# Kernel optimization log

Hardware: AMD Instinct MI355X
Metric: run time of the kernel (lower is better)

Reference implementation:

```python
import jax, jax.numpy as jnp
import numpy as np

N = 20000      # nodes
D_IN = 512     # input_dim
D_H = 256      # hyper_dim = input_dim // 2
C = 7          # class_num
E = 320000     # edges per class graph
E2 = 100000    # candidate pair list length
B = 8192       # batch of evaluated pairs (edge_id)
H3 = D_IN + C * D_H  # 2304, GatedNetwork / fc2 width
MIN = 1e-15
CURV = 1.0

def _norm(x):
    return jnp.maximum(jnp.linalg.norm(x, axis=-1, keepdims=True), MIN)

def artanh(x):
    x = jnp.clip(x, -1.0 + 1e-7, 1.0 - 1e-7)
    return 0.5 * (jnp.log1p(x) - jnp.log1p(-x))

def proj(x, c):
    # clip to inside the Poincare ball
    n = _norm(x)
    maxn = (1.0 - 4e-3) / jnp.sqrt(c)
    return jnp.where(n > maxn, x / n * maxn, x)

def expmap0(u, c):
    sc = jnp.sqrt(c); n = _norm(u)
    return jnp.tanh(sc * n) * u / (sc * n)

def logmap0(p, c):
    sc = jnp.sqrt(c); n = _norm(p)
    return artanh(sc * n) * p / (sc * n)

def mobius_add(x, y, c):
    x2 = jnp.sum(x * x, -1, keepdims=True)
    y2 = jnp.sum(y * y, -1, keepdims=True)
    xy = jnp.sum(x * y, -1, keepdims=True)
    num = (1 + 2 * c * xy + c * y2) * x + (1 - c * x2) * y
    den = 1 + 2 * c * xy + c * c * x2 * y2
    return num / jnp.maximum(den, MIN)

def mobius_matvec(m, x, c):
    sc = jnp.sqrt(c)
    xn = _norm(x)
    mx = x @ m.T
    mxn = _norm(mx)
    res = jnp.tanh(mxn / xn * artanh(sc * xn)) * mx / (mxn * sc)
    zero = jnp.all(mx == 0, axis=-1, keepdims=True)
    return jnp.where(zero, jnp.zeros((), mx.dtype), res)


def setup_inputs() -> dict:
    key = jax.random.key(0)
    ks = iter(jax.random.split(key, 48))
    def dense(shape, fan_in):
        return jax.random.normal(next(ks), shape, jnp.float32) * (1.0 / np.sqrt(fan_in))
    inp = {}
    inp['f1'] = jax.random.normal(next(ks), (N, D_IN), jnp.float32)
    inp['adj_src'] = jax.random.randint(next(ks), (C, E), 0, N)
    inp['adj_dst'] = jax.random.randint(next(ks), (C, E), 0, N)
    inp['adj_val'] = jax.random.uniform(next(ks), (C, E), jnp.float32) / 16.0  # ~row-normalized weights
    inp['edge_src'] = jax.random.randint(next(ks), (C, E), 0, N)
    inp['edge_dst'] = jax.random.randint(next(ks), (C, E), 0, N)
    inp['edge_index'] = jax.random.randint(next(ks), (2, E2), 0, N)
    inp['edge_id'] = jax.random.randint(next(ks), (B,), 0, E2)
    # per-class HypLinear
    inp['W_hyp'] = dense((C, D_H, D_IN), D_IN)
    inp['b_hyp'] = jnp.zeros((C, D_H), jnp.float32)
    # per-class HyperbolicDecoder linear
    inp['Wd'] = dense((C, D_H, D_H), D_H)
    inp['bd'] = jnp.zeros((C, D_H), jnp.float32)
    # per-class GIN MLP: lin1 -> BN -> tanh -> lin2
    inp['Wg1'] = dense((C, D_H, D_H), D_H)
    inp['bg1'] = jnp.zeros((C, D_H), jnp.float32)
    inp['gamma'] = jnp.ones((C, D_H), jnp.float32)
    inp['beta'] = jnp.zeros((C, D_H), jnp.float32)
    inp['Wg2'] = dense((C, D_H, D_H), D_H)
    inp['bg2'] = jnp.zeros((C, D_H), jnp.float32)
    # GatedInteractionNetwork
    inp['Wgate'] = dense((H3, H3), H3); inp['bgate'] = jnp.zeros((H3,), jnp.float32)
    inp['Wint'] = dense((H3, H3), H3); inp['bint'] = jnp.zeros((H3,), jnp.float32)
    inp['Wout'] = dense((H3, H3), H3); inp['bout'] = jnp.zeros((H3,), jnp.float32)
    # fc2 MLP head
    inp['Wf1'] = dense((H3 // 2, H3), H3); inp['bf1'] = jnp.zeros((H3 // 2,), jnp.float32)
    inp['Wf2'] = dense((H3 // 4, H3 // 2), H3 // 2); inp['bf2'] = jnp.zeros((H3 // 4,), jnp.float32)
    inp['Wf3'] = dense((C, H3 // 4), H3 // 4); inp['bf3'] = jnp.zeros((C,), jnp.float32)
    return inp


def reference(f1, adj_val, W_hyp, b_hyp, Wd, bd, Wg1, bg1, gamma, beta, Wg2, bg2,
              Wgate, bgate, Wint, bint, Wout, bout, Wf1, bf1, Wf2, bf2, Wf3, bf3,
              adj_src, adj_dst, edge_src, edge_dst, edge_index, edge_id):
    c = jnp.float32(CURV)
    # proj_tan0 is identity on the Poincare ball
    x_hyp = proj(expmap0(f1, c), c)
    outs = [f1]
    for i in range(C):
        # HypLinear: mobius matvec + hyperbolic bias
        res = proj(mobius_matvec(W_hyp[i], x_hyp, c), c)
        hb = proj(expmap0(b_hyp[i][None, :], c), c)
        res = proj(mobius_add(res, hb, c), c)
        # HypAgg: spmm(adj, logmap0(x)) then expmap0
        xt = logmap0(res, c)                     # [N, D_H]
        msg = adj_val[i][:, None] * xt[adj_src[i]]
        support = jax.ops.segment_sum(msg, adj_dst[i], num_segments=N)
        h = proj(expmap0(support, c), c)
        # HypAct: relu in tangent space at origin
        h = proj(expmap0(jax.nn.relu(logmap0(h, c)), c), c)
        # HyperbolicDecoder: logmap0 then euclidean linear
        d = logmap0(h, c) @ Wd[i].T + bd[i]
        # GIN (1 layer, eps=0): mlp(x + sum_neighbors x_j), mlp = lin->BN->tanh->lin
        agg = d + jax.ops.segment_sum(d[edge_src[i]], edge_dst[i], num_segments=N)
        z = agg @ Wg1[i].T + bg1[i]
        mu = jnp.mean(z, axis=0)
        var = jnp.var(z, axis=0)
        z = (z - mu) / jnp.sqrt(var + 1e-5) * gamma[i] + beta[i]
        z = jnp.tanh(z)
        outs.append(z @ Wg2[i].T + bg2[i])
    x = jnp.concatenate(outs, axis=1)            # [N, H3]
    nid = edge_index[:, edge_id]                 # [2, B]
    x1 = x[nid[0]]
    x2 = x[nid[1]]
    # GatedInteractionNetwork
    gate = jax.nn.sigmoid((x1 + x2) @ Wgate.T + bgate)
    gi = gate * jax.nn.relu((x1 * x2) @ Wint.T + bint)
    g = gi @ Wout.T + bout
    # fc2 head
    h1 = jax.nn.relu(g @ Wf1.T + bf1)
    h2 = jax.nn.relu(h1 @ Wf2.T + bf2)
    return h2 @ Wf3.T + bf3                      # [B, C]
```

## Files before the change

### kernel.cpp

```cpp
#include <hip/hip_runtime.h>
#include <math.h>

#define N_NODES 20000
#define D_INN   512
#define DH      256
#define NCH     7
#define NE      320000
#define NE2     100000
#define NB      8192
#define H3      2304
#define MAXN    0.996f
#define LOG2E   1.44269504f
#define NBUK    40
#define BSH     9

typedef unsigned short u16;
typedef __attribute__((ext_vector_type(8))) short bf16x8;
typedef __attribute__((ext_vector_type(4))) float f32x4;

__device__ __forceinline__ u16 f2b(float f) {
    unsigned int x = __float_as_uint(f);
    unsigned int r = (x + 0x7fffu + ((x >> 16) & 1u)) >> 16;
    return (u16)r;
}
__device__ __forceinline__ float b2f(u16 u) {
    return __uint_as_float(((unsigned int)u) << 16);
}
__device__ __forceinline__ float blo(unsigned int u) { return __uint_as_float(u << 16); }
__device__ __forceinline__ float bhi(unsigned int u) { return __uint_as_float(u & 0xffff0000u); }
__device__ __forceinline__ unsigned int pk2(float a, float b) {
    return (unsigned int)f2b(a) | ((unsigned int)f2b(b) << 16);
}

__device__ __forceinline__ float rcp_f(float x) { return __builtin_amdgcn_rcpf(x); }
__device__ __forceinline__ float exp2_f(float x) { return __builtin_amdgcn_exp2f(x); }
__device__ __forceinline__ float log2_f(float x) { return __builtin_amdgcn_logf(x); }
__device__ __forceinline__ float tanh_fast(float x) {
    float xc = fminf(fmaxf(x, -15.f), 15.f);
    float t = exp2_f(xc * (2.f * LOG2E));
    return (t - 1.f) * rcp_f(t + 1.f);
}
__device__ __forceinline__ float artanh_fast(float x) {
    x = fminf(fmaxf(x, -1.0f + 1e-7f), 1.0f - 1e-7f);
    return 0.34657359f * log2_f((1.f + x) * rcp_f(1.f - x));
}
__device__ __forceinline__ float sigmoid_fast(float x) {
    return rcp_f(1.f + exp2_f(-x * LOG2E));
}

__device__ __forceinline__ float wave_sum(float v) {
    #pragma unroll
    for (int off = 32; off > 0; off >>= 1) v += __shfl_xor(v, off, 64);
    return v;
}

__device__ __forceinline__ float block_sum256(float v) {
    __shared__ float sred[4];
    #pragma unroll
    for (int off = 32; off > 0; off >>= 1) v += __shfl_down(v, off, 64);
    int lane = threadIdx.x & 63;
    int w = threadIdx.x >> 6;
    if (lane == 0) sred[w] = v;
    __syncthreads();
    float tot = sred[0] + sred[1] + sred[2] + sred[3];
    __syncthreads();
    return tot;
}

__global__ void k_zero(float* __restrict__ p, int n) {
    int i = blockIdx.x * 256 + threadIdx.x;
    if (i < n) p[i] = 0.0f;
}
__global__ void k_izero(int* __restrict__ p, int n) {
    int i = blockIdx.x * 256 + threadIdx.x;
    if (i < n) p[i] = 0;
}

__global__ void k_f2b(const float* __restrict__ s, u16* __restrict__ d, int n4) {
    int i = blockIdx.x * 256 + threadIdx.x;
    int stride = gridDim.x * 256;
    for (; i < n4; i += stride) {
        float4 v = ((const float4*)s)[i];
        uint2 o; o.x = pk2(v.x, v.y); o.y = pk2(v.z, v.w);
        ((uint2*)d)[i] = o;
    }
}

__global__ void k_bias2(const float* __restrict__ a, const float* __restrict__ b,
                        float* __restrict__ o) {
    int i = blockIdx.x * 256 + threadIdx.x;
    if (i < H3) o[i] = a[i];
    else if (i < 2 * H3) o[i] = b[i - H3];
}

__global__ void k_gi(const u16* __restrict__ gate, const u16* __restrict__ tmp,
                     u16* __restrict__ out, int total4) {
    int i = blockIdx.x * 256 + threadIdx.x;
    int stride = gridDim.x * 256;
    for (; i < total4; i += stride) {
        uint2 g = ((const uint2*)gate)[i];
        uint2 t = ((const uint2*)tmp)[i];
        uint2 o;
        o.x = pk2(blo(g.x) * fmaxf(blo(t.x), 0.f), bhi(g.x) * fmaxf(bhi(t.x), 0.f));
        o.y = pk2(blo(g.y) * fmaxf(blo(t.y), 0.f), bhi(g.y) * fmaxf(bhi(t.y), 0.f));
        ((uint2*)out)[i] = o;
    }
}

__global__ void k_twd(const float* __restrict__ Wd, u16* __restrict__ Wdt) {
    __shared__ float tile[16][17];
    int z = blockIdx.z;
    int bx = blockIdx.x * 16, by = blockIdx.y * 16;
    int tx = threadIdx.x & 15, ty = threadIdx.x >> 4;
    tile[ty][tx] = Wd[(size_t)z * DH * DH + (size_t)(by + ty) * DH + bx + tx];
    __syncthreads();
    Wdt[(size_t)z * DH * DH + (size_t)(bx + ty) * DH + by + tx] = f2b(tile[tx][ty]);
}

__global__ void k_tr(const float* __restrict__ Win, u16* __restrict__ Wt) {
    __shared__ float tile[16][17];
    int bx = blockIdx.x * 16, by = blockIdx.y * 16;
    int tx = threadIdx.x & 15, ty = threadIdx.x >> 4;
    tile[ty][tx] = Win[(size_t)(by + ty) * H3 + bx + tx];
    __syncthreads();
    Wt[(size_t)(bx + ty) * H3 + by + tx] = f2b(tile[tx][ty]);
}

__global__ void k_bvec(const float* __restrict__ Wf1, const float* __restrict__ bout,
                       const float* __restrict__ bf1, float* __restrict__ bcomb) {
    int r = blockIdx.x * 4 + (threadIdx.x >> 6);
    int lane = threadIdx.x & 63;
    const float* row = Wf1 + (size_t)r * H3;
    float s = 0.f;
    for (int j = lane; j < H3; j += 64) s = fmaf(row[j], bout[j], s);
    s = wave_sum(s);
    if (lane == 0) bcomb[r] = s + bf1[r];
}

__global__ void k_cvec(const float* __restrict__ Wg1, const float* __restrict__ bd,
                       float* __restrict__ cvec) {
    int z = blockIdx.x, j = threadIdx.x;
    const float* row = Wg1 + (size_t)z * DH * DH + (size_t)j * DH;
    const float* b = bd + (size_t)z * DH;
    float s = 0.f;
    for (int k = 0; k < DH; ++k) s = fmaf(row[k], b[k], s);
    cvec[(size_t)z * DH + j] = s;
}

__global__ void k_hist2(const int* __restrict__ adjd, const int* __restrict__ edged,
                        int* __restrict__ cnt, int G) {
    int z = blockIdx.y;
    const int* dst = (z < G) ? adjd + (size_t)z * NE : edged + (size_t)(z - G) * NE;
    cnt += (size_t)z * N_NODES;
    int i = blockIdx.x * 256 + threadIdx.x;
    if (i < NE) atomicAdd(&cnt[dst[i]], 1);
}

__global__ void k_scan(int* __restrict__ cnt, int* __restrict__ rowptr) {
    int z = blockIdx.x;
    cnt += (size_t)z * N_NODES;
    rowptr += (size_t)z * (N_NODES + 1);
    __shared__ int part[256];
    int t = threadIdx.x;
    const int CH = (N_NODES + 255) / 256;
    int beg = t * CH;
    int end = beg + CH; if (end > N_NODES) end = N_NODES;
    int s = 0;
    for (int i = beg; i < end; ++i) s += cnt[i];
    part[t] = s;
    __syncthreads();
    for (int off = 1; off < 256; off <<= 1) {
        int v = (t >= off) ? part[t - off] : 0;
        __syncthreads();
        part[t] += v;
        __syncthreads();
    }
    int run = (t == 0) ? 0 : part[t - 1];
    for (int i = beg; i < end; ++i) {
        int c = cnt[i];
        rowptr[i] = run;
        cnt[i] = run;
        run += c;
    }
    if (t == 255) rowptr[N_NODES] = part[255];
}

__global__ void k_place2(const int* __restrict__ adjs, const int* __restrict__ adjd,
                         const float* __restrict__ adjv, const int* __restrict__ edges,
                         const int* __restrict__ edged, int* __restrict__ cursor,
                         uint2* __restrict__ padj, int* __restrict__ psrcE, int G) {
    int z = blockIdx.y;
    bool isadj = z < G;
    const int* src = isadj ? adjs + (size_t)z * NE : edges + (size_t)(z - G) * NE;
    const int* dst = isadj ? adjd + (size_t)z * NE : edged + (size_t)(z - G) * NE;
    cursor += (size_t)z * N_NODES;
    int i = blockIdx.x * 256 + threadIdx.x;
    if (i < NE) {
        int d = dst[i];
        int pos = atomicAdd(&cursor[d], 1);
        if (isadj) {
            uint2 p;
            p.x = (unsigned int)src[i];
            p.y = __float_as_uint(adjv[(size_t)z * NE + i]);
            padj[(size_t)z * NE + pos] = p;
        } else {
            psrcE[(size_t)(z - G) * NE + pos] = src[i];
        }
    }
}

__global__ void k_bcur(const int* __restrict__ rowptr, int* __restrict__ bcur, int G2) {
    int i = blockIdx.x * 256 + threadIdx.x;
    if (i < G2 * NBUK) {
        int z = i / NBUK, b = i - z * NBUK;
        bcur[i] = rowptr[(size_t)z * (N_NODES + 1) + (b << BSH)];
    }
}

__global__ void k_binA(const int* __restrict__ adjs, const int* __restrict__ adjd,
                       const float* __restrict__ adjv, const int* __restrict__ edges,
                       const int* __restrict__ edged, int* __restrict__ bcur,
                       uint2* __restrict__ scrA, unsigned int* __restrict__ scrE, int G) {
    int z = blockIdx.y;
    bool isadj = z < G;
    const int* src = isadj ? adjs + (size_t)z * NE : edges + (size_t)(z - G) * NE;
    const int* dst = isadj ? adjd + (size_t)z * NE : edged + (size_t)(z - G) * NE;
    __shared__ int hcnt[NBUK];
    __shared__ int gbase[NBUK];
    int t = threadIdx.x;
    int i = blockIdx.x * 256 + t;
    if (t < NBUK) hcnt[t] = 0;
    __syncthreads();
    int s = 0, d = 0, buk = 0, rank = 0;
    bool valid = i < NE;
    if (valid) {
        s = src[i]; d = dst[i];
        buk = d >> BSH;
        rank = atomicAdd(&hcnt[buk], 1);
    }
    __syncthreads();
    if (t < NBUK && hcnt[t] > 0)
        gbase[t] = atomicAdd(&bcur[z * NBUK + t], hcnt[t]);
    __syncthreads();
    if (valid) {
        int pos = gbase[buk] + rank;
        unsigned int sd = (unsigned int)s | ((unsigned int)d << 15);
        if (isadj) {
            uint2 p; p.x = sd; p.y = __float_as_uint(adjv[(size_t)z * NE + i]);
            scrA[(size_t)z * NE + pos] = p;
        } else {
            scrE[(size_t)(z - G) * NE + pos] = sd;
        }
    }
}

__global__ void k_placeB(const int* __restrict__ rowptr, const uint2* __restrict__ scrA,
                         const unsigned int* __restrict__ scrE, uint2* __restrict__ padj,
                         int* __restrict__ psrcE, int G) {
    int z = blockIdx.y;
    int b = blockIdx.x;
    bool isadj = z < G;
    const int* rp = rowptr + (size_t)z * (N_NODES + 1);
    __shared__ int cur[512];
    int t = threadIdx.x;
    int n0 = b << BSH;
    for (int k = t; k < 512; k += 256) {
        int node = n0 + k;
        cur[k] = (node < N_NODES) ? rp[node] : 0;
    }
    __syncthreads();
    int beg = rp[n0];
    int nend = n0 + 512; if (nend > N_NODES) nend = N_NODES;
    int end = rp[nend];
    if (isadj) {
        const uint2* sc = scrA + (size_t)z * NE;
        uint2* out = padj + (size_t)z * NE;
        for (int i = beg + t; i < end; i += 256) {
            uint2 p = sc[i];
            int d = (int)((p.x >> 15) & 0x7fffu);
            int pos = atomicAdd(&cur[d - n0], 1);
            uint2 o; o.x = p.x & 0x7fffu; o.y = p.y;
            out[pos] = o;
        }
    } else {
        const unsigned int* sc = scrE + (size_t)(z - G) * NE;
        int* out = psrcE + (size_t)(z - G) * NE;
        for (int i = beg + t; i < end; i += 256) {
            unsigned int p = sc[i];
            int d = (int)((p >> 15) & 0x7fffu);
            int pos = atomicAdd(&cur[d - n0], 1);
            out[pos] = (int)(p & 0x7fffu);
        }
    }
}

__global__ void k_expmap_proj_in(const float* __restrict__ f1,
                                 u16* __restrict__ xhyp, float* __restrict__ xhn) {
    int r = blockIdx.x, t = threadIdx.x;
    const float* u = f1 + (size_t)r * D_INN;
    float v0 = u[t], v1 = u[t + 256];
    float ss = block_sum256(v0 * v0 + v1 * v1);
    float nraw = sqrtf(ss);
    float n = fmaxf(nraw, 1e-15f);
    float c = tanh_fast(n) * rcp_f(n);
    float ny = c * nraw;
    float np = fmaxf(ny, 1e-15f);
    float s = (np > MAXN) ? MAXN * rcp_f(np) : 1.0f;
    float cs = c * s;
    u16* o = xhyp + (size_t)r * D_INN;
    o[t] = f2b(cs * v0);
    o[t + 256] = f2b(cs * v1);
    if (t == 0) xhn[r] = fminf(np, MAXN);
}

__global__ void k_hb(const float* __restrict__ b_hyp,
                     float* __restrict__ hb, float* __restrict__ hb2) {
    int i = blockIdx.x, t = threadIdx.x;
    float v = b_hyp[i * DH + t];
    float ss = block_sum256(v * v);
    float nraw = sqrtf(ss);
    float n = fmaxf(nraw, 1e-15f);
    float c = tanh_fast(n) * rcp_f(n);
    float ny = c * nraw;
    float np = fmaxf(ny, 1e-15f);
    float s = (np > MAXN) ? MAXN * rcp_f(np) : 1.0f;
    float hv = c * s * v;
    hb[i * DH + t] = hv;
    float s2 = block_sum256(hv * hv);
    if (t == 0) hb2[i] = s2;
}

__global__ void k_rowfuse1(u16* __restrict__ T, const float* __restrict__ xhn,
                           const float* __restrict__ hb, const float* __restrict__ hb2) {
    int z = blockIdx.y;
    int n = blockIdx.x * 4 + (threadIdx.x >> 6);
    int lane = threadIdx.x & 63;
    u16* row = T + ((size_t)z * N_NODES + n) * DH;
    const float* hbz = hb + (size_t)z * DH;
    uint2 u = *(const uint2*)(row + lane * 4);
    float m0 = blo(u.x), m1 = bhi(u.x), m2 = blo(u.y), m3 = bhi(u.y);
    float ss = wave_sum(m0 * m0 + m1 * m1 + m2 * m2 + m3 * m3);
    float mxn_raw = sqrtf(ss);
    float mxn = fmaxf(mxn_raw, 1e-15f);
    float xn = xhn[n];
    float tt = tanh_fast(mxn * rcp_f(xn) * artanh_fast(xn));
    float coef = tt * rcp_f(mxn);
    float nres = coef * mxn_raw;
    float np = fmaxf(nres, 1e-15f);
    float s1 = (np > MAXN) ? MAXN * rcp_f(np) : 1.0f;
    float cs = coef * s1;
    float r0 = cs * m0, r1 = cs * m1, r2 = cs * m2, r3 = cs * m3;
    float n1 = fminf(np, MAXN);
    float4 hv = *(const float4*)(hbz + lane * 4);
    float xy = wave_sum(r0 * hv.x + r1 * hv.y + r2 * hv.z + r3 * hv.w);
    float x2 = n1 * n1, y2 = hb2[z];
    float ca = 1.0f + 2.0f * xy + y2;
    float cb = 1.0f - x2;
    float rden = rcp_f(fmaxf(1.0f + 2.0f * xy + x2 * y2, 1e-15f));
    float o0 = (ca * r0 + cb * hv.x) * rden;
    float o1 = (ca * r1 + cb * hv.y) * rden;
    float o2 = (ca * r2 + cb * hv.z) * rden;
    float o3 = (ca * r3 + cb * hv.w) * rden;
    float no2 = wave_sum(o0 * o0 + o1 * o1 + o2 * o2 + o3 * o3);
    float nop = fmaxf(sqrtf(no2), 1e-15f);
    float s2 = (nop > MAXN) ? MAXN * rcp_f(nop) : 1.0f;
    float n2 = fminf(nop, MAXN);
    float fin = artanh_fast(n2) * rcp_f(n2) * s2;
    uint2 o; o.x = pk2(fin * o0, fin * o1); o.y = pk2(fin * o2, fin * o3);
    *(uint2*)(row + lane * 4) = o;
}

__global__ void k_gather_fuse2(const int* __restrict__ rowptr, const uint2* __restrict__ padj,
                               const u16* __restrict__ xt, u16* __restrict__ out) {
    int z = blockIdx.y;
    rowptr += (size_t)z * (N_NODES + 1);
    padj += (size_t)z * NE;
    xt += (size_t)z * N_NODES * DH;
    out += (size_t)z * N_NODES * DH;
    int n = blockIdx.x * 4 + (threadIdx.x >> 6);
    int lane = threadIdx.x & 63;
    int beg = rowptr[n], end = rowptr[n + 1];
    float a0 = 0.f, a1 = 0.f, a2 = 0.f, a3 = 0.f;
    float b0 = 0.f, b1 = 0.f, b2 = 0.f, b3 = 0.f;
    int i = beg;
    for (; i + 2 <= end; i += 2) {
        uint2 p0 = padj[i];
        uint2 p1 = padj[i + 1];
        uint2 x0 = *(const uint2*)(xt + (size_t)p0.x * DH + lane * 4);
        uint2 x1 = *(const uint2*)(xt + (size_t)p1.x * DH + lane * 4);
        float v0 = __uint_as_float(p0.y), v1 = __uint_as_float(p1.y);
        a0 = fmaf(v0, blo(x0.x), a0);
        a1 = fmaf(v0, bhi(x0.x), a1);
        a2 = fmaf(v0, blo(x0.y), a2);
        a3 = fmaf(v0, bhi(x0.y), a3);
        b0 = fmaf(v1, blo(x1.x), b0);
        b1 = fmaf(v1, bhi(x1.x), b1);
        b2 = fmaf(v1, blo(x1.y), b2);
        b3 = fmaf(v1, bhi(x1.y), b3);
    }
    if (i < end) {
        uint2 p = padj[i];
        uint2 x0 = *(const uint2*)(xt + (size_t)p.x * DH + lane * 4);
        float v = __uint_as_float(p.y);
        a0 = fmaf(v, blo(x0.x), a0);
        a1 = fmaf(v, bhi(x0.x), a1);
        a2 = fmaf(v, blo(x0.y), a2);
        a3 = fmaf(v, bhi(x0.y), a3);
    }
    a0 += b0; a1 += b1; a2 += b2; a3 += b3;
    float ss = wave_sum(a0 * a0 + a1 * a1 + a2 * a2 + a3 * a3);
    float nraw = sqrtf(ss);
    float n_ = fmaxf(nraw, 1e-15f);
    float c1 = tanh_fast(n_) * rcp_f(n_);
    float nh = c1 * nraw;
    float np1 = fmaxf(nh, 1e-15f);
    float s1 = (np1 > MAXN) ? MAXN * rcp_f(np1) : 1.0f;
    float n1 = fminf(np1, MAXN);
    float cu = artanh_fast(n1) * rcp_f(n1) * s1 * c1;
    float u0 = fmaxf(cu * a0, 0.f), u1 = fmaxf(cu * a1, 0.f);
    float u2 = fmaxf(cu * a2, 0.f), u3 = fmaxf(cu * a3, 0.f);
    float ss2 = wave_sum(u0 * u0 + u1 * u1 + u2 * u2 + u3 * u3);
    float n2raw = sqrtf(ss2);
    float n2 = fmaxf(n2raw, 1e-15f);
    float c3 = tanh_fast(n2) * rcp_f(n2);
    float ne = c3 * n2raw;
    float np3 = fmaxf(ne, 1e-15f);
    float s3 = (np3 > MAXN) ? MAXN * rcp_f(np3) : 1.0f;
    float n3 = fminf(np3, MAXN);
    float cf = artanh_fast(n3) * rcp_f(n3) * s3 * c3;
    uint2 o; o.x = pk2(cf * u0, cf * u1); o.y = pk2(cf * u2, cf * u3);
    *(uint2*)(out + (size_t)n * DH + lane * 4) = o;
}

__global__ void k_gather_add(const int* __restrict__ rowptr, const int* __restrict__ psrc,
                             const u16* __restrict__ d, u16* __restrict__ out) {
    int z = blockIdx.y;
    rowptr += (size_t)z * (N_NODES + 1);
    psrc += (size_t)z * NE;
    d += (size_t)z * N_NODES * DH;
    out += (size_t)z * N_NODES * DH;
    int n = blockIdx.x * 4 + (threadIdx.x >> 6);
    int lane = threadIdx.x & 63;
    int beg = rowptr[n], end = rowptr[n + 1];
    uint2 u0v = *(const uint2*)(d + (size_t)n * DH + lane * 4);
    float a0 = blo(u0v.x), a1 = bhi(u0v.x), a2 = blo(u0v.y), a3 = bhi(u0v.y);
    float b0 = 0.f, b1 = 0.f, b2 = 0.f, b3 = 0.f;
    int i = beg;
    for (; i + 2 <= end; i += 2) {
        int s0 = psrc[i], s1 = psrc[i + 1];
        uint2 x0 = *(const uint2*)(d + (size_t)s0 * DH + lane * 4);
        uint2 x1 = *(const uint2*)(d + (size_t)s1 * DH + lane * 4);
        a0 += blo(x0.x); a1 += bhi(x0.x); a2 += blo(x0.y); a3 += bhi(x0.y);
        b0 += blo(x1.x); b1 += bhi(x1.x); b2 += blo(x1.y); b3 += bhi(x1.y);
    }
    if (i < end) {
        int s0 = psrc[i];
        uint2 x0 = *(const uint2*)(d + (size_t)s0 * DH + lane * 4);
        a0 += blo(x0.x); a1 += bhi(x0.x); a2 += blo(x0.y); a3 += bhi(x0.y);
    }
    a0 += b0; a1 += b1; a2 += b2; a3 += b3;
    uint2 o; o.x = pk2(a0, a1); o.y = pk2(a2, a3);
    *(uint2*)(out + (size_t)n * DH + lane * 4) = o;
}

__global__ void k_colstats(const u16* __restrict__ zp,
                           float* __restrict__ csum, float* __restrict__ csq) {
    int z = blockIdx.y;
    zp += (size_t)z * N_NODES * DH;
    csum += (size_t)z * DH;
    csq += (size_t)z * DH;
    int t = threadIdx.x;
    int r0 = blockIdx.x * 100;
    float s = 0.0f, q = 0.0f;
    for (int r = r0; r < r0 + 100; ++r) {
        float v = b2f(zp[(size_t)r * DH + t]);
        s += v;
        q += v * v;
    }
    atomicAdd(&csum[t], s);
    atomicAdd(&csq[t], q);
}

__global__ void k_normtanh_v(u16* __restrict__ zp, const float* __restrict__ csum,
                             const float* __restrict__ csq, const float* __restrict__ gamma,
                             const float* __restrict__ beta, int total4) {
    const float inv_n = 1.0f / N_NODES;
    int i = blockIdx.x * 256 + threadIdx.x;
    int stride = gridDim.x * 256;
    for (; i < total4; i += stride) {
        int e0 = i * 4;
        int z = e0 / (N_NODES * DH);
        int j0 = e0 & (DH - 1);
        int zb = z * DH + j0;
        uint2 u = ((uint2*)zp)[i];
        float v[4] = {blo(u.x), bhi(u.x), blo(u.y), bhi(u.y)};
        #pragma unroll
        for (int k = 0; k < 4; ++k) {
            float mu = csum[zb + k] * inv_n;
            float var = csq[zb + k] * inv_n - mu * mu;
            float inv = __builtin_amdgcn_rsqf(var + 1e-5f);
            v[k] = tanh_fast((v[k] - mu) * inv * gamma[zb + k] + beta[zb + k]);
        }
        uint2 o; o.x = pk2(v[0], v[1]); o.y = pk2(v[2], v[3]);
        ((uint2*)zp)[i] = o;
    }
}

__global__ void k_pair0(const int* __restrict__ ei, const int* __restrict__ eid,
                        const float* __restrict__ f1, u16* __restrict__ S,
                        u16* __restrict__ P) {
    int b = blockIdx.x, t = threadIdx.x;
    int e = eid[b];
    int n0 = ei[e], n1 = ei[NE2 + e];
    float2 a = *(const float2*)(f1 + (size_t)n0 * D_INN + t * 2);
    float2 c = *(const float2*)(f1 + (size_t)n1 * D_INN + t * 2);
    ((unsigned int*)(S + (size_t)b * H3))[t] = pk2(a.x + c.x, a.y + c.y);
    ((unsigned int*)(P + (size_t)b * H3))[t] = pk2(a.x * c.x, a.y * c.y);
}

__global__ void k_gather_ch(const int* __restrict__ ei, const int* __restrict__ eid,
                            const u16* __restrict__ zch, u16* __restrict__ S,
                            u16* __restrict__ P, int col0base) {
    int z = blockIdx.y;
    const u16* zp = zch + (size_t)z * N_NODES * DH;
    int col0 = col0base + z * DH;
    int b = blockIdx.x * 4 + (threadIdx.x >> 6);
    int lane = threadIdx.x & 63;
    int e = eid[b];
    int n0 = ei[e], n1 = ei[NE2 + e];
    uint2 ua = *(const uint2*)(zp + (size_t)n0 * DH + lane * 4);
    uint2 ub = *(const uint2*)(zp + (size_t)n1 * DH + lane * 4);
    float a0 = blo(ua.x), a1 = bhi(ua.x), a2 = blo(ua.y), a3 = bhi(ua.y);
    float c0 = blo(ub.x), c1 = bhi(ub.x), c2 = blo(ub.y), c3 = bhi(ub.y);
    uint2 so; so.x = pk2(a0 + c0, a1 + c1); so.y = pk2(a2 + c2, a3 + c3);
    uint2 po; po.x = pk2(a0 * c0, a1 * c1); po.y = pk2(a2 * c2, a3 * c3);
    *(uint2*)(S + (size_t)b * H3 + col0 + lane * 4) = so;
    *(uint2*)(P + (size_t)b * H3 + col0 + lane * 4) = po;
}

__global__ void k_final(const u16* __restrict__ h2, const float* __restrict__ Wf3,
                        const float* __restrict__ bf3, float* __restrict__ out) {
    int r = blockIdx.x, t = threadIdx.x;
    const u16* hr = h2 + (size_t)r * 576;
    float acc[7] = {0, 0, 0, 0, 0, 0, 0};
    for (int cb = t; cb < 576; cb += 64) {
        float h = b2f(hr[cb]);
        #pragma unroll
        for (int o = 0; o < 7; ++o) acc[o] = fmaf(h, Wf3[o * 576 + cb], acc[o]);
    }
    #pragma unroll
    for (int o = 0; o < 7; ++o) {
        #pragma unroll
        for (int off = 32; off > 0; off >>= 1) acc[o] += __shfl_down(acc[o], off, 64);
    }
    if (t == 0) {
        #pragma unroll
        for (int o = 0; o < 7; ++o) out[(size_t)r * 7 + o] = acc[o] + bf3[o];
    }
}

template <int EP>
__global__ __launch_bounds__(512, 4) void k_gemm_mfma(
    const u16* __restrict__ A, const u16* __restrict__ W,
    const float* __restrict__ bias, void* __restrict__ outv,
    const int* __restrict__ rpe, const float* __restrict__ cvec,
    int M, int N, int K, size_t sA, size_t sW, size_t sC, int sBias) {
    __shared__ short As[8192];
    __shared__ short Ws[8192];
    const int gx = gridDim.x, gy = gridDim.y;
    const int plane = gx * gy;
    const int total = plane * gridDim.z;
    const int orig = (blockIdx.z * gy + blockIdx.y) * gx + blockIdx.x;
    const int q8 = total >> 3, r8 = total & 7, xcd = orig & 7;
    const int wg = (xcd < r8 ? xcd * (q8 + 1) : r8 * (q8 + 1) + (xcd - r8) * q8) + (orig >> 3);
    const int z = wg / plane;
    const int rem = wg - z * plane;
    const int row0 = (rem / gx) * 128, col0 = (rem % gx) * 128;
    A += (size_t)z * sA;
    W += (size_t)z * sW;
    const size_t zC = (size_t)z * sC;
    const int* rp = (EP == 7) ? rpe + (size_t)z * (N_NODES + 1) : nullptr;
    const float* cv = (EP == 7) ? cvec + (size_t)z * DH : nullptr;
    const int t = threadIdx.x;
    const int lane = t & 63;
    const int w = t >> 6;
    const int wr = w >> 2;
    const int wc = w & 3;
    const int sr8 = lane >> 3;
    const int csrc = (lane & 7) ^ sr8;
    int gr[2], gc[2];
    #pragma unroll
    for (int p = 0; p < 2; ++p) {
        int rb = w + p * 8;
        gr[p] = row0 + rb * 8 + sr8; if (gr[p] >= M) gr[p] = M - 1;
        gc[p] = col0 + rb * 8 + sr8; if (gc[p] >= N) gc[p] = N - 1;
    }
    const int fr = lane & 15, fq4 = lane >> 4;
    f32x4 acc[4][2] = {};
    for (int k0 = 0; k0 < K; k0 += 64) {
        #pragma unroll
        for (int p = 0; p < 2; ++p) {
            int rb = w + p * 8;
            __builtin_amdgcn_global_load_lds(
                (const __attribute__((address_space(1))) unsigned int*)(A + (size_t)gr[p] * K + k0 + csrc * 8),
                (__attribute__((address_space(3))) unsigned int*)(As + rb * 512), 16, 0, 0);
            __builtin_amdgcn_global_load_lds(
                (const __attribute__((address_space(1))) unsigned int*)(W + (size_t)gc[p] * K + k0 + csrc * 8),
                (__attribute__((address_space(3))) unsigned int*)(Ws + rb * 512), 16, 0, 0);
        }
        __syncthreads();
        bf16x8 af[4][2], bfr[2][2];
        #pragma unroll
        for (int m = 0; m < 4; ++m) {
            int ar = wr * 64 + m * 16 + fr;
            #pragma unroll
            for (int kk = 0; kk < 2; ++kk) {
                int q = kk * 4 + fq4;
                af[m][kk] = *(const bf16x8*)(As + ar * 64 + ((q ^ (ar & 7)) * 8));
            }
        }
        #pragma unroll
        for (int n = 0; n < 2; ++n) {
            int br = wc * 32 + n * 16 + fr;
            #pragma unroll
            for (int kk = 0; kk < 2; ++kk) {
                int q = kk * 4 + fq4;
                bfr[n][kk] = *(const bf16x8*)(Ws + br * 64 + ((q ^ (br & 7)) * 8));
            }
        }
        #pragma unroll
        for (int m = 0; m < 4; ++m)
            #pragma unroll
            for (int n = 0; n < 2; ++n)
                #pragma unroll
                for (int kk = 0; kk < 2; ++kk)
                    acc[m][n] = __builtin_amdgcn_mfma_f32_16x16x32_bf16(
                        af[m][kk], bfr[n][kk], acc[m][n], 0, 0, 0);
        __syncthreads();
    }
    const int cl = lane & 15, rh = (lane >> 4) * 4;
    #pragma unroll
    for (int m = 0; m < 4; ++m) {
        float indf[4];
        if (EP == 7) {
            #pragma unroll
            for (int r = 0; r < 4; ++r) {
                int row = row0 + wr * 64 + m * 16 + rh + r;
                if (row >= M) row = M - 1;
                indf[r] = 1.0f + (float)(rp[row + 1] - rp[row]);
            }
        }
        #pragma unroll
        for (int n = 0; n < 2; ++n) {
            int col = col0 + wc * 32 + n * 16 + cl;
            if (col >= N) continue;
            float bv = bias ? bias[z * sBias + col] : 0.0f;
            float cvc = (EP == 7) ? cv[col] : 0.0f;
            #pragma unroll
            for (int r = 0; r < 4; ++r) {
                int row = row0 + wr * 64 + m * 16 + rh + r;
                if (row >= M) continue;
                float v = acc[m][n][r] + bv;
                size_t idx = zC + (size_t)row * N + col;
                if (EP == 2) ((u16*)outv)[idx] = f2b(sigmoid_fast(v));
                if (EP == 3) ((u16*)outv)[idx] = f2b(fmaxf(v, 0.0f));
                if (EP == 5) ((u16*)outv)[idx] = f2b(v);
                if (EP == 6) ((float*)outv)[idx] = fmaxf(v, 0.0f);
                if (EP == 7) ((u16*)outv)[idx] = f2b(v + indf[r] * cvc);
                if (EP == 8) ((u16*)outv)[idx] = (z == 0) ? f2b(sigmoid_fast(v)) : f2b(v);
            }
        }
    }
}

static inline void gemm_b(int ep, const u16* A, const u16* W, const float* bias, void* out,
                          const int* rpe, const float* cvec,
                          int M, int N, int K, int Z,
                          size_t sA, size_t sW, size_t sC, int sBias, hipStream_t st) {
    dim3 g((N + 127) / 128, (M + 127) / 128, Z);
    switch (ep) {
        case 2: k_gemm_mfma<2><<<g, 512, 0, st>>>(A, W, bias, out, rpe, cvec, M, N, K, sA, sW, sC, sBias); break;
        case 3: k_gemm_mfma<3><<<g, 512, 0, st>>>(A, W, bias, out, rpe, cvec, M, N, K, sA, sW, sC, sBias); break;
        case 5: k_gemm_mfma<5><<<g, 512, 0, st>>>(A, W, bias, out, rpe, cvec, M, N, K, sA, sW, sC, sBias); break;
        case 6: k_gemm_mfma<6><<<g, 512, 0, st>>>(A, W, bias, out, rpe, cvec, M, N, K, sA, sW, sC, sBias); break;
        case 7: k_gemm_mfma<7><<<g, 512, 0, st>>>(A, W, bias, out, rpe, cvec, M, N, K, sA, sW, sC, sBias); break;
        case 8: k_gemm_mfma<8><<<g, 512, 0, st>>>(A, W, bias, out, rpe, cvec, M, N, K, sA, sW, sC, sBias); break;
    }
}

static inline void conv_w(const float* s, u16* d, size_t n, hipStream_t st) {
    int n4 = (int)(n / 4);
    int grid = (n4 + 255) / 256;
    if (grid > 2048) grid = 2048;
    k_f2b<<<grid, 256, 0, st>>>(s, d, n4);
}

extern "C" void kernel_launch(void* const* d_in, const int* in_sizes, int n_in, void* d_out,
                              int out_size, void* d_ws, size_t ws_size, hipStream_t stream) {
    const float* f1 = (const float*)d_in[0];
    const int* adj_src = (const int*)d_in[1];
    const int* adj_dst = (const int*)d_in[2];
    const float* adj_val = (const float*)d_in[3];
    const int* edge_src = (const int*)d_in[4];
    const int* edge_dst = (const int*)d_in[5];
    const int* edge_index = (const int*)d_in[6];
    const int* edge_id = (const int*)d_in[7];
    const float* W_hyp = (const float*)d_in[8];
    const float* b_hyp = (const float*)d_in[9];
    const float* Wd = (const float*)d_in[10];
    const float* bd = (const float*)d_in[11];
    const float* Wg1 = (const float*)d_in[12];
    const float* bg1 = (const float*)d_in[13];
    const float* gamma = (const float*)d_in[14];
    const float* beta = (const float*)d_in[15];
    const float* Wg2 = (const float*)d_in[16];
    const float* bg2 = (const float*)d_in[17];
    const float* Wgate = (const float*)d_in[18];
    const float* bgate = (const float*)d_in[19];
    const float* Wint = (const float*)d_in[20];
    const float* bint = (const float*)d_in[21];
    const float* Wout = (const float*)d_in[22];
    const float* bout = (const float*)d_in[23];
    const float* Wf1 = (const float*)d_in[24];
    const float* bf1 = (const float*)d_in[25];
    const float* Wf2 = (const float*)d_in[26];
    const float* bf2 = (const float*)d_in[27];
    const float* Wf3 = (const float*)d_in[28];
    const float* bf3 = (const float*)d_in[29];
    float* outp = (float*)d_out;

    const bool single = ws_size >= 253400000ull;
    const int ngroups = single ? 1 : 2;
    const int GM = single ? 7 : 4;
    int g0s[2] = {0, 4};
    int gns[2] = {GM, 3};

    char* base = (char*)d_ws;
    size_t off = 0;
    auto alloc = [&](size_t bytes) -> char* {
        char* p = base + off;
        off += (bytes + 255) & ~(size_t)255;
        return p;
    };
    u16* Whyp_b = (u16*)alloc((size_t)NCH * DH * D_INN * 2);
    u16* Wc_b   = (u16*)alloc((size_t)NCH * DH * DH * 2);
    u16* Wg1_b  = (u16*)alloc((size_t)NCH * DH * DH * 2);
    u16* Wg2_b  = (u16*)alloc((size_t)NCH * DH * DH * 2);
    u16* Wgate_b = (u16*)alloc((size_t)H3 * H3 * 2);
    u16* Wint_b  = (u16*)alloc((size_t)H3 * H3 * 2);
    u16* Wcomb_b = (u16*)alloc((size_t)1152 * H3 * 2);
    u16* Wf2_b   = (u16*)alloc((size_t)576 * 1152 * 2);
    u16* S_b = (u16*)alloc((size_t)NB * H3 * 2);
    u16* P_b = (u16*)alloc((size_t)NB * H3 * 2);
    const size_t NDB = (size_t)N_NODES * DH;
    u16* buf1 = (u16*)alloc((size_t)GM * NDB * 2);
    u16* buf2 = (u16*)alloc((size_t)GM * NDB * 2);
    u16* xhyp_b = single ? buf2 : (u16*)alloc((size_t)N_NODES * D_INN * 2);
    int* cntC; int* rowptrC; uint2* padjC; int* psrcE;
    uint2* scrA = nullptr; unsigned int* scrE = nullptr;
    if (single) {
        padjC = (uint2*)S_b;
        psrcE = (int*)((char*)S_b + (size_t)GM * NE * 8);
        cntC = (int*)P_b;
        rowptrC = (int*)((char*)P_b + (size_t)2 * GM * N_NODES * 4);
        size_t rp_end = (size_t)2 * GM * N_NODES * 4 + (size_t)2 * GM * (N_NODES + 1) * 4;
        rp_end = (rp_end + 63) & ~(size_t)63;
        scrA = (uint2*)((char*)P_b + rp_end);
        scrE = (unsigned int*)((char*)scrA + (size_t)GM * NE * 8);
    } else {
        cntC = (int*)alloc((size_t)2 * GM * N_NODES * 4);
        rowptrC = (int*)alloc((size_t)2 * GM * (N_NODES + 1) * 4);
        padjC = (uint2*)alloc((size_t)GM * NE * 8);
        psrcE = (int*)alloc((size_t)GM * NE * 4);
    }
    float* xhn = (float*)alloc((size_t)N_NODES * 4);
    float* hb = (float*)alloc((size_t)NCH * DH * 4);
    float* hb2 = (float*)alloc(NCH * 4);
    float* csum = (float*)alloc((size_t)GM * DH * 4);
    float* csq = (float*)alloc((size_t)GM * DH * 4);
    float* cvec_d = (float*)alloc((size_t)NCH * DH * 4);
    float* bias2 = (float*)alloc((size_t)2 * H3 * 4);
    float* bcomb = (float*)alloc((size_t)1152 * 4);
    int* bcur = (int*)alloc((size_t)2 * NCH * NBUK * 4);
    u16* WoutT_b = buf1;
    u16* Wf1_b = buf1 + (size_t)H3 * H3;
    u16* Wdt_b = Wf1_b + (size_t)1152 * H3;
    u16* GT = buf1;
    u16* h2b = buf2;

    const int EG = (NE + 255) / 256;

    conv_w(W_hyp, Whyp_b, (size_t)NCH * DH * D_INN, stream);
    conv_w(Wg1, Wg1_b, (size_t)NCH * DH * DH, stream);
    conv_w(Wg2, Wg2_b, (size_t)NCH * DH * DH, stream);
    conv_w(Wgate, Wgate_b, (size_t)H3 * H3, stream);
    conv_w(Wint, Wint_b, (size_t)H3 * H3, stream);
    conv_w(Wf1, Wf1_b, (size_t)1152 * H3, stream);
    conv_w(Wf2, Wf2_b, (size_t)576 * 1152, stream);
    k_bias2<<<(2 * H3 + 255) / 256, 256, 0, stream>>>(bgate, bint, bias2);
    k_twd<<<dim3(16, 16, NCH), 256, 0, stream>>>(Wd, Wdt_b);
    gemm_b(5, Wg1_b, Wdt_b, nullptr, Wc_b, nullptr, nullptr,
           DH, DH, DH, NCH, (size_t)DH * DH, (size_t)DH * DH, (size_t)DH * DH, 0, stream);
    k_cvec<<<NCH, 256, 0, stream>>>(Wg1, bd, cvec_d);
    k_tr<<<dim3(144, 144), 256, 0, stream>>>(Wout, WoutT_b);
    gemm_b(5, Wf1_b, WoutT_b, nullptr, Wcomb_b, nullptr, nullptr,
           1152, H3, H3, 1, 0, 0, 0, 0, stream);
    k_bvec<<<1152 / 4, 256, 0, stream>>>(Wf1, bout, bf1, bcomb);

    k_expmap_proj_in<<<N_NODES, 256, 0, stream>>>(f1, xhyp_b, xhn);
    k_hb<<<NCH, 256, 0, stream>>>(b_hyp, hb, hb2);
    if (!single) k_pair0<<<NB, 256, 0, stream>>>(edge_index, edge_id, f1, S_b, P_b);

    for (int gi = 0; gi < ngroups; ++gi) {
        const int g0 = g0s[gi], G = gns[gi];
        const size_t eoff = (size_t)g0 * NE;
        const int G2 = 2 * G;
        const int* rpE = rowptrC + (size_t)G * (N_NODES + 1);
        k_izero<<<(G2 * N_NODES + 255) / 256, 256, 0, stream>>>(cntC, G2 * N_NODES);
        k_hist2<<<dim3(EG, G2), 256, 0, stream>>>(adj_dst + eoff, edge_dst + eoff, cntC, G);
        k_scan<<<G2, 256, 0, stream>>>(cntC, rowptrC);
        if (single) {
            k_bcur<<<(G2 * NBUK + 255) / 256, 256, 0, stream>>>(rowptrC, bcur, G2);
            k_binA<<<dim3(EG, G2), 256, 0, stream>>>(adj_src, adj_dst, adj_val,
                                                     edge_src, edge_dst, bcur,
                                                     scrA, scrE, G);
            k_placeB<<<dim3(NBUK, G2), 256, 0, stream>>>(rowptrC, scrA, scrE,
                                                         padjC, psrcE, G);
        } else {
            k_place2<<<dim3(EG, G2), 256, 0, stream>>>(adj_src + eoff, adj_dst + eoff,
                                                       adj_val + eoff, edge_src + eoff,
                                                       edge_dst + eoff, cntC, padjC,
                                                       psrcE, G);
        }
        gemm_b(5, xhyp_b, Whyp_b + (size_t)g0 * DH * D_INN, nullptr, buf1, nullptr,
               nullptr, N_NODES, DH, D_INN, G, 0, (size_t)DH * D_INN, NDB, 0, stream);
        k_rowfuse1<<<dim3(N_NODES / 4, G), 256, 0, stream>>>(buf1, xhn, hb + g0 * DH, hb2 + g0);
        k_gather_fuse2<<<dim3(N_NODES / 4, G), 256, 0, stream>>>(rowptrC, padjC, buf1, buf2);
        k_gather_add<<<dim3(N_NODES / 4, G), 256, 0, stream>>>(rpE, psrcE, buf2, buf1);
        gemm_b(7, buf1, Wc_b + (size_t)g0 * DH * DH, bg1 + g0 * DH, buf2,
               rpE, cvec_d + (size_t)g0 * DH, N_NODES, DH, DH, G,
               NDB, (size_t)DH * DH, NDB, DH, stream);
        k_zero<<<(2 * GM * DH + 255) / 256, 256, 0, stream>>>(csum, 2 * GM * DH);
        k_colstats<<<dim3(200, G), 256, 0, stream>>>(buf2, csum, csq);
        {
            int total4 = (int)(G * NDB / 4);
            int blocks = (total4 + 255) / 256;
            if (blocks > 2048) blocks = 2048;
            k_normtanh_v<<<blocks, 256, 0, stream>>>(buf2, csum, csq, gamma + g0 * DH,
                                                     beta + g0 * DH, total4);
        }
        gemm_b(5, buf2, Wg2_b + (size_t)g0 * DH * DH, bg2 + g0 * DH, buf1, nullptr,
               nullptr, N_NODES, DH, DH, G, NDB, (size_t)DH * DH, NDB, DH, stream);
        if (!single)
            k_gather_ch<<<dim3(NB / 4, G), 256, 0, stream>>>(edge_index, edge_id, buf1,
                                                             S_b, P_b, D_INN + g0 * DH);
    }
    if (single) {
        k_pair0<<<NB, 256, 0, stream>>>(edge_index, edge_id, f1, S_b, P_b);
        k_gather_ch<<<dim3(NB / 4, 7), 256, 0, stream>>>(edge_index, edge_id, buf1,
                                                         S_b, P_b, D_INN);
    }

    gemm_b(8, S_b, Wgate_b, bias2, GT, nullptr, nullptr, NB, H3, H3, 2,
           (size_t)NB * H3, (size_t)H3 * H3, (size_t)NB * H3, H3, stream);
    {
        int total4 = NB * H3 / 4;
        int blocks = (total4 + 255) / 256;
        if (blocks > 2048) blocks = 2048;
        k_gi<<<blocks, 256, 0, stream>>>(GT, GT + (size_t)NB * H3, S_b, total4);
    }
    gemm_b(3, S_b, Wcomb_b, bcomb, buf1, nullptr, nullptr, NB, 1152, H3, 1, 0, 0, 0, 0, stream);
    gemm_b(3, buf1, Wf2_b, bf2, h2b, nullptr, nullptr, NB, 576, 1152, 1, 0, 0, 0, 0, stream);
    k_final<<<NB, 64, 0, stream>>>(h2b, Wf3, bf3, outp);
}
```

Measured before the change: 1.460 ms.

## Unroll gather loops by four and remap GEMM tile order for column reuse

The two CSR gather kernels now process four neighbours per iteration with four independent accumulator sets, so more row loads are in flight and latency is better hidden. The MFMA GEMM's workgroup-to-tile mapping changes when the column grid is a multiple of three: consecutive workgroups sweep a group of three column tiles down all rows, aiming for better L2 reuse of the weight tiles. The cost is higher register pressure in the gather kernels and a different cache access pattern in the GEMM.

```diff
diff --git a/kernel.cpp b/kernel.cpp
--- a/kernel.cpp
+++ b/kernel.cpp
@@ -382,52 +382,70 @@
     int beg = rowptr[n], end = rowptr[n + 1];
     float a0 = 0.f, a1 = 0.f, a2 = 0.f, a3 = 0.f;
     float b0 = 0.f, b1 = 0.f, b2 = 0.f, b3 = 0.f;
+    float c0 = 0.f, c1 = 0.f, c2 = 0.f, c3 = 0.f;
+    float d0 = 0.f, d1 = 0.f, d2 = 0.f, d3 = 0.f;
     int i = beg;
-    for (; i + 2 <= end; i += 2) {
+    for (; i + 4 <= end; i += 4) {
+        uint2 p0 = padj[i];
+        uint2 p1 = padj[i + 1];
+        uint2 p2 = padj[i + 2];
+        uint2 p3 = padj[i + 3];
+        uint2 x0 = *(const uint2*)(xt + (size_t)p0.x * DH + lane * 4);
+        uint2 x1 = *(const uint2*)(xt + (size_t)p1.x * DH + lane * 4);
+        uint2 x2 = *(const uint2*)(xt + (size_t)p2.x * DH + lane * 4);
+        uint2 x3 = *(const uint2*)(xt + (size_t)p3.x * DH + lane * 4);
+        float v0 = __uint_as_float(p0.y), v1 = __uint_as_float(p1.y);
+        float v2 = __uint_as_float(p2.y), v3 = __uint_as_float(p3.y);
+        a0 = fmaf(v0, blo(x0.x), a0); a1 = fmaf(v0, bhi(x0.x), a1);
+        a2 = fmaf(v0, blo(x0.y), a2); a3 = fmaf(v0, bhi(x0.y), a3);
+        b0 = fmaf(v1, blo(x1.x), b0); b1 = fmaf(v1, bhi(x1.x), b1);
+        b2 = fmaf(v1, blo(x1.y), b2); b3 = fmaf(v1, bhi(x1.y), b3);
+        c0 = fmaf(v2, blo(x2.x), c0); c1 = fmaf(v2, bhi(x2.x), c1);
+        c2 = fmaf(v2, blo(x2.y), c2); c3 = fmaf(v2, bhi(x2.y), c3);
+        d0 = fmaf(v3, blo(x3.x), d0); d1 = fmaf(v3, bhi(x3.x), d1);
+        d2 = fmaf(v3, blo(x3.y), d2); d3 = fmaf(v3, bhi(x3.y), d3);
+    }
+    if (i + 2 <= end) {
         uint2 p0 = padj[i];
         uint2 p1 = padj[i + 1];
         uint2 x0 = *(const uint2*)(xt + (size_t)p0.x * DH + lane * 4);
         uint2 x1 = *(const uint2*)(xt + (size_t)p1.x * DH + lane * 4);
         float v0 = __uint_as_float(p0.y), v1 = __uint_as_float(p1.y);
-        a0 = fmaf(v0, blo(x0.x), a0);
-        a1 = fmaf(v0, bhi(x0.x), a1);
-        a2 = fmaf(v0, blo(x0.y), a2);
-        a3 = fmaf(v0, bhi(x0.y), a3);
-        b0 = fmaf(v1, blo(x1.x), b0);
-        b1 = fmaf(v1, bhi(x1.x), b1);
-        b2 = fmaf(v1, blo(x1.y), b2);
-        b3 = fmaf(v1, bhi(x1.y), b3);
+        a0 = fmaf(v0, blo(x0.x), a0); a1 = fmaf(v0, bhi(x0.x), a1);
+        a2 = fmaf(v0, blo(x0.y), a2); a3 = fmaf(v0, bhi(x0.y), a3);
+        b0 = fmaf(v1, blo(x1.x), b0); b1 = fmaf(v1, bhi(x1.x), b1);
+        b2 = fmaf(v1, blo(x1.y), b2); b3 = fmaf(v1, bhi(x1.y), b3);
+        i += 2;
     }
     if (i < end) {
         uint2 p = padj[i];
         uint2 x0 = *(const uint2*)(xt + (size_t)p.x * DH + lane * 4);
         float v = __uint_as_float(p.y);
-        a0 = fmaf(v, blo(x0.x), a0);
-        a1 = fmaf(v, bhi(x0.x), a1);
-        a2 = fmaf(v, blo(x0.y), a2);
-        a3 = fmaf(v, bhi(x0.y), a3);
-    }
-    a0 += b0; a1 += b1; a2 += b2; a3 += b3;
+        a0 = fmaf(v, blo(x0.x), a0); a1 = fmaf(v, bhi(x0.x), a1);
+        a2 = fmaf(v, blo(x0.y), a2); a3 = fmaf(v, bhi(x0.y), a3);
+    }
+    a0 += b0 + c0 + d0; a1 += b1 + c1 + d1;
+    a2 += b2 + c2 + d2; a3 += b3 + c3 + d3;
     float ss = wave_sum(a0 * a0 + a1 * a1 + a2 * a2 + a3 * a3);
     float nraw = sqrtf(ss);
     float n_ = fmaxf(nraw, 1e-15f);
-    float c1 = tanh_fast(n_) * rcp_f(n_);
-    float nh = c1 * nraw;
+    float cc1 = tanh_fast(n_) * rcp_f(n_);
+    float nh = cc1 * nraw;
     float np1 = fmaxf(nh, 1e-15f);
     float s1 = (np1 > MAXN) ? MAXN * rcp_f(np1) : 1.0f;
     float n1 = fminf(np1, MAXN);
-    float cu = artanh_fast(n1) * rcp_f(n1) * s1 * c1;
+    float cu = artanh_fast(n1) * rcp_f(n1) * s1 * cc1;
     float u0 = fmaxf(cu * a0, 0.f), u1 = fmaxf(cu * a1, 0.f);
     float u2 = fmaxf(cu * a2, 0.f), u3 = fmaxf(cu * a3, 0.f);
     float ss2 = wave_sum(u0 * u0 + u1 * u1 + u2 * u2 + u3 * u3);
     float n2raw = sqrtf(ss2);
     float n2 = fmaxf(n2raw, 1e-15f);
-    float c3 = tanh_fast(n2) * rcp_f(n2);
-    float ne = c3 * n2raw;
+    float cc3 = tanh_fast(n2) * rcp_f(n2);
+    float ne = cc3 * n2raw;
     float np3 = fmaxf(ne, 1e-15f);
     float s3 = (np3 > MAXN) ? MAXN * rcp_f(np3) : 1.0f;
     float n3 = fminf(np3, MAXN);
-    float cf = artanh_fast(n3) * rcp_f(n3) * s3 * c3;
+    float cf = artanh_fast(n3) * rcp_f(n3) * s3 * cc3;
     uint2 o; o.x = pk2(cf * u0, cf * u1); o.y = pk2(cf * u2, cf * u3);
     *(uint2*)(out + (size_t)n * DH + lane * 4) = o;
 }
@@ -445,20 +463,35 @@
     uint2 u0v = *(const uint2*)(d + (size_t)n * DH + lane * 4);
     float a0 = blo(u0v.x), a1 = bhi(u0v.x), a2 = blo(u0v.y), a3 = bhi(u0v.y);
     float b0 = 0.f, b1 = 0.f, b2 = 0.f, b3 = 0.f;
+    float c0 = 0.f, c1 = 0.f, c2 = 0.f, c3 = 0.f;
+    float e0 = 0.f, e1 = 0.f, e2 = 0.f, e3 = 0.f;
     int i = beg;
-    for (; i + 2 <= end; i += 2) {
+    for (; i + 4 <= end; i += 4) {
+        int s0 = psrc[i], s1 = psrc[i + 1], s2 = psrc[i + 2], s3 = psrc[i + 3];
+        uint2 x0 = *(const uint2*)(d + (size_t)s0 * DH + lane * 4);
+        uint2 x1 = *(const uint2*)(d + (size_t)s1 * DH + lane * 4);
+        uint2 x2 = *(const uint2*)(d + (size_t)s2 * DH + lane * 4);
+        uint2 x3 = *(const uint2*)(d + (size_t)s3 * DH + lane * 4);
+        a0 += blo(x0.x); a1 += bhi(x0.x); a2 += blo(x0.y); a3 += bhi(x0.y);
+        b0 += blo(x1.x); b1 += bhi(x1.x); b2 += blo(x1.y); b3 += bhi(x1.y);
+        c0 += blo(x2.x); c1 += bhi(x2.x); c2 += blo(x2.y); c3 += bhi(x2.y);
+        e0 += blo(x3.x); e1 += bhi(x3.x); e2 += blo(x3.y); e3 += bhi(x3.y);
+    }
+    if (i + 2 <= end) {
         int s0 = psrc[i], s1 = psrc[i + 1];
         uint2 x0 = *(const uint2*)(d + (size_t)s0 * DH + lane * 4);
         uint2 x1 = *(const uint2*)(d + (size_t)s1 * DH + lane * 4);
         a0 += blo(x0.x); a1 += bhi(x0.x); a2 += blo(x0.y); a3 += bhi(x0.y);
         b0 += blo(x1.x); b1 += bhi(x1.x); b2 += blo(x1.y); b3 += bhi(x1.y);
+        i += 2;
     }
     if (i < end) {
         int s0 = psrc[i];
         uint2 x0 = *(const uint2*)(d + (size_t)s0 * DH + lane * 4);
         a0 += blo(x0.x); a1 += bhi(x0.x); a2 += blo(x0.y); a3 += bhi(x0.y);
     }
-    a0 += b0; a1 += b1; a2 += b2; a3 += b3;
+    a0 += b0 + c0 + e0; a1 += b1 + c1 + e1;
+    a2 += b2 + c2 + e2; a3 += b3 + c3 + e3;
     uint2 o; o.x = pk2(a0, a1); o.y = pk2(a2, a3);
     *(uint2*)(out + (size_t)n * DH + lane * 4) = o;
 }
@@ -573,9 +606,24 @@
     const int orig = (blockIdx.z * gy + blockIdx.y) * gx + blockIdx.x;
     const int q8 = total >> 3, r8 = total & 7, xcd = orig & 7;
     const int wg = (xcd < r8 ? xcd * (q8 + 1) : r8 * (q8 + 1) + (xcd - r8) * q8) + (orig >> 3);
-    const int z = wg / plane;
-    const int rem = wg - z * plane;
-    const int row0 = (rem / gx) * 128, col0 = (rem % gx) * 128;
+    int z_, row0_, col0_;
+    if (gx % 3 == 0) {
+        int cc = wg % 3;
+        int y = (wg / 3) % gy;
+        int rest = wg / (3 * gy);
+        int TC = gx / 3;
+        int tc = rest % TC;
+        z_ = rest / TC;
+        row0_ = y * 128;
+        col0_ = (tc * 3 + cc) * 128;
+    } else {
+        z_ = wg / plane;
+        int rem = wg - z_ * plane;
+        row0_ = (rem / gx) * 128;
+        col0_ = (rem % gx) * 128;
+    }
+    const int z = z_;
+    const int row0 = row0_, col0 = col0_;
     A += (size_t)z * sA;
     W += (size_t)z * sW;
     const size_t zC = (size_t)z * sC;
```

After: 1.414 ms. -3.1%, faster.
